# Kernel optimization log

Hardware: AMD Instinct MI355X
Metric: run time of the kernel (lower is better)

The kernel has to match this reference:

```python
import jax, jax.numpy as jnp
import numpy as np

GRID = 30
S = GRID * GRID            # 900 cells
D = 512                    # embed_dim
HQ = 8                     # query heads
HKV = 2                    # kv heads (GQA)
DH = D // HQ               # 64 head dim
T = 16                     # history length


def _rope_pairwise_1d(x, pos, inv_freq):
    """RoPE on adjacent pairs. x: (L,H,d), pos: (L,), inv_freq: (d//2,)."""
    theta = pos[:, None] * inv_freq[None, :]          # (L, d//2)
    cos = jnp.cos(theta)[:, None, :]                  # (L,1,d//2)
    sin = jnp.sin(theta)[:, None, :]
    xr, xi = x[..., 0::2], x[..., 1::2]               # even/odd pairs (= view(L,H,-1,2))
    out = jnp.stack((xr * cos - xi * sin, xr * sin + xi * cos), axis=-1)
    return out.reshape(x.shape)


def _rope_2d(x, coords_xy, inv_x, inv_y):
    """2D RoPE: first half rotated by x-coord, second half by y-coord."""
    d_axis = x.shape[-1] // 2
    x_part = _rope_pairwise_1d(x[..., :d_axis], coords_xy[:, 0], inv_x)
    y_part = _rope_pairwise_1d(x[..., d_axis:], coords_xy[:, 1], inv_y)
    return jnp.concatenate((x_part, y_part), axis=-1)


def setup_inputs() -> dict:
    key = jax.random.key(0)
    ks = jax.random.split(key, 7)
    sc = 1.0 / np.sqrt(D)
    return {
        "static_grid": jax.random.normal(ks[0], (GRID, GRID, D), jnp.float32),
        "history_seq": jax.random.normal(ks[1], (T, GRID, GRID, D), jnp.float32),
        "init_embed": jax.random.normal(ks[2], (D,), jnp.float32),
        "Wq": jax.random.normal(ks[3], (D, D), jnp.float32) * sc,
        "Wk": jax.random.normal(ks[4], (HKV * DH, D), jnp.float32) * sc,
        "Wv": jax.random.normal(ks[5], (HKV * DH, D), jnp.float32) * sc,
        "Wo": jax.random.normal(ks[6], (D, D), jnp.float32) * sc,
    }


def reference(static_grid, history_seq, init_embed, Wq, Wk, Wv, Wo):
    dtype = static_grid.dtype
    quarter, half = DH // 4, DH // 2
    inv_2d = 1.0 / (10000.0 ** (jnp.arange(quarter, dtype=dtype) / quarter))  # (dh//4,)
    inv_1d = 1.0 / (10000.0 ** (jnp.arange(half, dtype=dtype) / half))        # (dh//2,)

    gy, gx = jnp.meshgrid(jnp.arange(GRID), jnp.arange(GRID), indexing="ij")
    coords = jnp.stack((gy, gx), axis=-1).reshape(S, 2).astype(dtype)          # (S,2)

    cur = static_grid.reshape(S, D)                    # current frame tokens
    hist = history_seq.reshape(T * S, D)               # per-cell histories
    # token order: [learnable_init, cell_histories (t=0..T-1), current_grid]
    tokens = jnp.concatenate((init_embed[None, :], hist, cur), axis=0)  # (Lkv, D)

    tok_pos = jnp.concatenate((
        jnp.zeros((1,), dtype),
        jnp.repeat(jnp.arange(T, dtype=dtype), S),
        jnp.full((S,), T, dtype=dtype),
    ))                                                  # (Lkv,) temporal positions
    tok_coords = jnp.concatenate((
        jnp.zeros((1, 2), dtype),
        jnp.tile(coords, (T, 1)),
        coords,
    ), axis=0)                                          # (Lkv,2)

    # projections (queries only for the current frame; output is the updated frame)
    q = (cur @ Wq.T).reshape(S, HQ, DH)
    k = (tokens @ Wk.T).reshape(-1, HKV, DH)
    v = (tokens @ Wv.T).reshape(-1, HKV, DH)

    # fused temporal(1D) + spatial(2D) RoPE on q and k
    q = _rope_2d(_rope_pairwise_1d(q, jnp.full((S,), T, dtype=dtype), inv_1d), coords, inv_2d, inv_2d)
    k = _rope_2d(_rope_pairwise_1d(k, tok_pos, inv_1d), tok_coords, inv_2d, inv_2d)

    # grouped-query attention: expand kv heads
    g = HQ // HKV
    k = jnp.repeat(k, g, axis=1)                        # (Lkv, HQ, DH)
    v = jnp.repeat(v, g, axis=1)

    scores = jnp.einsum("qhd,khd->hqk", q, k) / jnp.sqrt(jnp.asarray(DH, dtype))

    # pedestal mask: attend to init + own temporal column + all current cells
    cell = jnp.arange(S)
    hist_cell = jnp.tile(cell, T)                       # (T*S,)
    mask = jnp.concatenate((
        jnp.ones((S, 1), bool),
        cell[:, None] == hist_cell[None, :],
        jnp.ones((S, S), bool),
    ), axis=1)                                          # (S, Lkv)
    scores = jnp.where(mask[None], scores, jnp.finfo(dtype).min)

    attn = jax.nn.softmax(scores, axis=-1)
    out = jnp.einsum("hqk,khd->qhd", attn, v).reshape(S, D)
    return (out @ Wo.T).reshape(GRID, GRID, D)
```

## Files before the change

### kernel.cpp

```cpp
#include <hip/hip_runtime.h>
#include <math.h>

static constexpr int GRIDN = 30;
static constexpr int S    = 900;
static constexpr int D    = 512;
static constexpr int HQ   = 8;
static constexpr int HKV  = 2;
static constexpr int T    = 16;
static constexpr int NTOK = 1 + T*S + S;
static constexpr int CUR0 = 1 + T*S;

static constexpr int THROWS = 15360;
static constexpr int VTC    = 960;
static constexpr int PBS    = 952;

typedef _Float16 half8  __attribute__((ext_vector_type(8)));
typedef _Float16 half4  __attribute__((ext_vector_type(4)));
typedef __fp16   fp16x2 __attribute__((ext_vector_type(2)));
typedef float    floatx4 __attribute__((ext_vector_type(4)));

#define MFMA16(a,b,c) __builtin_amdgcn_mfma_f32_16x16x32_f16((a),(b),(c),0,0,0)

#if defined(__has_builtin)
#if __has_builtin(__builtin_amdgcn_fdot2)
#define HAVE_FDOT2 1
#endif
#endif

__device__ __forceinline__ half8 to_half8(float4 a, float4 b) {
    half8 h;
    h[0]=(_Float16)a.x; h[1]=(_Float16)a.y; h[2]=(_Float16)a.z; h[3]=(_Float16)a.w;
    h[4]=(_Float16)b.x; h[5]=(_Float16)b.y; h[6]=(_Float16)b.z; h[7]=(_Float16)b.w;
    return h;
}

__device__ __forceinline__ half8 cvt8(float4 a, float4 b) {
    const fp16x2 p0 = __builtin_amdgcn_cvt_pkrtz(a.x, a.y);
    const fp16x2 p1 = __builtin_amdgcn_cvt_pkrtz(a.z, a.w);
    const fp16x2 p2 = __builtin_amdgcn_cvt_pkrtz(b.x, b.y);
    const fp16x2 p3 = __builtin_amdgcn_cvt_pkrtz(b.z, b.w);
    half8 h;
    h[0]=(_Float16)p0[0]; h[1]=(_Float16)p0[1];
    h[2]=(_Float16)p1[0]; h[3]=(_Float16)p1[1];
    h[4]=(_Float16)p2[0]; h[5]=(_Float16)p2[1];
    h[6]=(_Float16)p3[0]; h[7]=(_Float16)p3[1];
    return h;
}

__global__ __launch_bounds__(256) void prep_w(
    const float* __restrict__ Wq, const float* __restrict__ Wk,
    const float* __restrict__ Wv, const float* __restrict__ Wo,
    _Float16* __restrict__ Wqh, _Float16* __restrict__ Whkv,
    _Float16* __restrict__ Woh)
{
    const size_t i8 = ((size_t)blockIdx.x * 256 + threadIdx.x) * 8;
    const float* src; _Float16* dst; size_t off;
    if (i8 < 262144)      { src = Wq; dst = Wqh;          off = i8; }
    else if (i8 < 327680) { src = Wk; dst = Whkv;         off = i8 - 262144; }
    else if (i8 < 393216) { src = Wv; dst = Whkv + 65536; off = i8 - 327680; }
    else                  { src = Wo; dst = Woh;          off = i8 - 393216; }
    const float4 f0 = *(const float4*)(src + off);
    const float4 f1 = *(const float4*)(src + off + 4);
    *(half8*)(dst + off) = to_half8(f0, f1);
}

__global__ __launch_bounds__(256) void proj(
    const float* __restrict__ init_e, const float* __restrict__ hist,
    const float* __restrict__ cur,
    const _Float16* __restrict__ Whkv, const _Float16* __restrict__ Wqh,
    _Float16* __restrict__ Kh, _Float16* __restrict__ Vh,
    _Float16* __restrict__ Vt, _Float16* __restrict__ Qh)
{
    const int tid = threadIdx.x;
    const int w = tid >> 6, lane = tid & 63;
    const int r = lane & 15, kb = lane >> 4;
    const int bx = blockIdx.x;
    const bool isQ = (bx >= 479);

    int l0, n0;
    const _Float16* B;
    if (!isQ) { l0 = bx * 32; B = Whkv; n0 = 0; }
    else {
        const int qb = bx - 479;
        l0 = CUR0 + (qb >> 1) * 32;
        B = Wqh; n0 = (qb & 1) * 256;
    }

    const float* ap[2];
    #pragma unroll
    for (int mt = 0; mt < 2; ++mt) {
        int l = l0 + mt*16 + r;
        if (l >= NTOK) l = 0;
        const float* row = (l == 0) ? init_e
                         : (l <= T*S ? hist + (size_t)(l-1)*512
                                     : cur  + (size_t)(l-CUR0)*512);
        ap[mt] = row + kb*8;
    }
    const _Float16* bp[4];
    #pragma unroll
    for (int nt = 0; nt < 4; ++nt)
        bp[nt] = B + (size_t)(n0 + w*64 + nt*16 + r) * 512 + kb*8;

    floatx4 acc[2][4] = {};
    #pragma unroll 2
    for (int k0 = 0; k0 < 512; k0 += 32) {
        half8 a[2], b[4];
        #pragma unroll
        for (int mt = 0; mt < 2; ++mt) {
            const float4 f0 = *(const float4*)(ap[mt] + k0);
            const float4 f1 = *(const float4*)(ap[mt] + k0 + 4);
            a[mt] = cvt8(f0, f1);
        }
        #pragma unroll
        for (int nt = 0; nt < 4; ++nt) b[nt] = *(const half8*)(bp[nt] + k0);
        #pragma unroll
        for (int mt = 0; mt < 2; ++mt)
            #pragma unroll
            for (int nt = 0; nt < 4; ++nt)
                acc[mt][nt] = MFMA16(a[mt], b[nt], acc[mt][nt]);
    }

    const float LN1E4 = 9.210340371976184f;
    float inv1[4], inv2[4]; int jj[4];
    #pragma unroll
    for (int nt = 0; nt < 4; ++nt) {
        const int cl = nt*16 + r;
        jj[nt] = cl >> 1;
        inv1[nt] = __expf(-(float)jj[nt]        * (LN1E4 / 32.f));
        inv2[nt] = __expf(-(float)(jj[nt] & 15) * (LN1E4 / 16.f));
    }

    if (!isQ) {
        if (w < 2) {
            #pragma unroll
            for (int mt = 0; mt < 2; ++mt)
                #pragma unroll
                for (int i = 0; i < 4; ++i) {
                    const int l = l0 + mt*16 + kb*4 + i;
                    float pos, cy, cx;
                    if (l == 0) { pos = 0.f; cy = 0.f; cx = 0.f; }
                    else if (l <= T*S) {
                        const int j2 = l - 1;
                        const int t_ = j2 / S;
                        const int cell = j2 - t_ * S;
                        pos = (float)t_;
                        cy = (float)(cell / GRIDN); cx = (float)(cell % GRIDN);
                    } else {
                        const int cell = l - CUR0;
                        pos = (float)T;
                        cy = (float)(cell / GRIDN); cx = (float)(cell % GRIDN);
                    }
                    #pragma unroll
                    for (int nt = 0; nt < 4; ++nt) {
                        const float own = acc[mt][nt][i];
                        const float oth = __shfl_xor(own, 1);
                        const float c2 = (jj[nt] < 16) ? cy : cx;
                        const float theta = pos * inv1[nt] + c2 * inv2[nt];
                        float sn, cs; __sincosf(theta, &sn, &cs);
                        const int cl = nt*16 + r;
                        const float o = ((cl & 1) == 0) ? (own * cs - oth * sn)
                                                        : (oth * sn + own * cs);
                        if (l < NTOK) Kh[(size_t)l * 128 + w*64 + cl] = (_Float16)o;
                    }
                }
        } else {
            #pragma unroll
            for (int mt = 0; mt < 2; ++mt)
                #pragma unroll
                for (int nt = 0; nt < 4; ++nt) {
                    const int d = nt*16 + r;
                    #pragma unroll
                    for (int i = 0; i < 4; ++i) {
                        const int l = l0 + mt*16 + kb*4 + i;
                        if (l >= NTOK) continue;
                        const _Float16 hv = (_Float16)acc[mt][nt][i];
                        Vh[(size_t)l * 128 + (w-2)*64 + d] = hv;
                        const int cc = l - CUR0;
                        if (cc >= 0 && cc < S)
                            Vt[((size_t)(w-2)*64 + d) * VTC + cc] = hv;
                    }
                }
        }
    } else {
        #pragma unroll
        for (int mt = 0; mt < 2; ++mt)
            #pragma unroll
            for (int i = 0; i < 4; ++i) {
                const int l = l0 + mt*16 + kb*4 + i;
                const int s = l - CUR0;
                const float cy = (float)(s / GRIDN), cx = (float)(s % GRIDN);
                #pragma unroll
                for (int nt = 0; nt < 4; ++nt) {
                    const float own = acc[mt][nt][i];
                    const float oth = __shfl_xor(own, 1);
                    const float c2 = (jj[nt] < 16) ? cy : cx;
                    const float theta = 16.f * inv1[nt] + c2 * inv2[nt];
                    float sn, cs; __sincosf(theta, &sn, &cs);
                    const int cl = nt*16 + r;
                    const float o = ((cl & 1) == 0) ? (own * cs - oth * sn)
                                                    : (oth * sn + own * cs);
                    if (s < S)
                        Qh[(size_t)s * 512 + n0 + w*64 + cl] = (_Float16)(o * 0.125f);
                }
            }
    }
}

__global__ __launch_bounds__(256) void attn_f16(
    const _Float16* __restrict__ Qh, const _Float16* __restrict__ Kh,
    const _Float16* __restrict__ Vt, const _Float16* __restrict__ Vh,
    _Float16* __restrict__ Oh)
{
    __shared__ _Float16 pb[16][PBS];
    __shared__ float ex[16][20];
    __shared__ float wpm[4][16], wps[4][16];
    __shared__ float rowm[16], rowinv[16];
    __shared__ float Oe[16][68];

    const int q0  = blockIdx.x * 16;
    const int h   = blockIdx.y;
    const int kvh = h >> 2;
    const int tid = threadIdx.x;
    const int w = tid >> 6, lane = tid & 63;
    const int r = lane & 15, g = lane >> 4;

    {
        const int er = tid & 15;
        const int s  = q0 + er;
        const int ss = (s < S) ? s : 0;
        const _Float16* qp = Qh + (size_t)(q0 + er) * 512 + h * 64;
        for (int e = tid >> 4; e < 17; e += 16) {
            const int l = (e == 0) ? 0 : (1 + (e - 1) * S + ss);
            const _Float16* kp = Kh + (size_t)l * 128 + kvh * 64;
            float acc = 0.f;
            #pragma unroll
            for (int d8 = 0; d8 < 8; ++d8) {
                const half8 qv = *(const half8*)(qp + d8 * 8);
                const half8 kv = *(const half8*)(kp + d8 * 8);
#ifdef HAVE_FDOT2
                #pragma unroll
                for (int p_ = 0; p_ < 4; ++p_) {
                    fp16x2 qq; qq[0] = (__fp16)qv[2*p_]; qq[1] = (__fp16)qv[2*p_+1];
                    fp16x2 kk; kk[0] = (__fp16)kv[2*p_]; kk[1] = (__fp16)kv[2*p_+1];
                    acc = __builtin_amdgcn_fdot2(qq, kk, acc, false);
                }
#else
                #pragma unroll
                for (int q_ = 0; q_ < 8; ++q_)
                    acc += (float)qv[q_] * (float)kv[q_];
#endif
            }
            ex[er][e] = acc;
        }
    }

    half8 qa[2];
    #pragma unroll
    for (int ks = 0; ks < 2; ++ks)
        qa[ks] = *(const half8*)(Qh + (size_t)(q0 + r) * 512 + h * 64 + ks * 32 + g * 8);

    floatx4 qacc[15];
    #pragma unroll
    for (int t = 0; t < 15; ++t) {
        const int nt = w + 4 * t;
        floatx4 a = {0.f, 0.f, 0.f, 0.f};
        if (nt <= 56) {
            const _Float16* kp = Kh + (size_t)(CUR0 + nt * 16 + r) * 128 + kvh * 64 + g * 8;
            a = MFMA16(qa[0], *(const half8*)kp, a);
            a = MFMA16(qa[1], *(const half8*)(kp + 32), a);
        }
        qacc[t] = a;
    }

    float pm[4] = {-1e30f, -1e30f, -1e30f, -1e30f};
    #pragma unroll
    for (int t = 0; t < 15; ++t) {
        const int nt = w + 4 * t;
        const bool valid = (nt <= 56) && !((nt == 56) && (r >= 4));
        #pragma unroll
        for (int i = 0; i < 4; ++i)
            if (valid) pm[i] = fmaxf(pm[i], qacc[t][i]);
    }
    #pragma unroll
    for (int m = 1; m < 16; m <<= 1)
        #pragma unroll
        for (int i = 0; i < 4; ++i)
            pm[i] = fmaxf(pm[i], __shfl_xor(pm[i], m));
    if (r == 0)
        #pragma unroll
        for (int i = 0; i < 4; ++i) wpm[w][g * 4 + i] = pm[i];
    __syncthreads();

    if (tid < 16) {
        float m = fmaxf(fmaxf(wpm[0][tid], wpm[1][tid]), fmaxf(wpm[2][tid], wpm[3][tid]));
        #pragma unroll
        for (int e = 0; e < 17; ++e) m = fmaxf(m, ex[tid][e]);
        rowm[tid] = m;
    }
    __syncthreads();

    {
        const int er = tid & 15;
        for (int e = tid >> 4; e < 17; e += 16)
            ex[er][e] = __expf(ex[er][e] - rowm[er]);
    }
    pb[tid >> 4][912 + (tid & 15)] = (_Float16)0.f;

    float ps[4] = {0.f, 0.f, 0.f, 0.f};
    #pragma unroll
    for (int t = 0; t < 15; ++t) {
        const int nt = w + 4 * t;
        if (nt <= 56) {
            const int c = nt * 16 + r;
            const bool masked = (nt == 56) && (r >= 4);
            #pragma unroll
            for (int i = 0; i < 4; ++i) {
                const int row = g * 4 + i;
                const float e = masked ? 0.f : __expf(qacc[t][i] - rowm[row]);
                ps[i] += e;
                pb[row][c] = (_Float16)e;
            }
        }
    }
    #pragma unroll
    for (int m = 1; m < 16; m <<= 1)
        #pragma unroll
        for (int i = 0; i < 4; ++i) ps[i] += __shfl_xor(ps[i], m);
    if (r == 0)
        #pragma unroll
        for (int i = 0; i < 4; ++i) wps[w][g * 4 + i] = ps[i];
    __syncthreads();

    if (tid < 16) {
        float s_ = wps[0][tid] + wps[1][tid] + wps[2][tid] + wps[3][tid];
        #pragma unroll
        for (int e = 0; e < 17; ++e) s_ += ex[tid][e];
        rowinv[tid] = 1.f / s_;
    }
    __syncthreads();

    {
        const int er = tid & 15, gg = tid >> 4;
        const int s  = q0 + er;
        const int ss = (s < S) ? s : 0;
        float o0 = 0.f, o1 = 0.f, o2 = 0.f, o3 = 0.f;
        for (int e = 0; e < 17; ++e) {
            const int l = (e == 0) ? 0 : (1 + (e - 1) * S + ss);
            const float p = ex[er][e];
            const half4 v = *(const half4*)(Vh + (size_t)l * 128 + kvh * 64 + gg * 4);
            o0 = fmaf(p, (float)v[0], o0); o1 = fmaf(p, (float)v[1], o1);
            o2 = fmaf(p, (float)v[2], o2); o3 = fmaf(p, (float)v[3], o3);
        }
        *(float4*)&Oe[er][gg * 4] = make_float4(o0, o1, o2, o3);
    }

    const int d0 = w * 16;
    floatx4 oa = {0.f, 0.f, 0.f, 0.f};
    const _Float16* vrow = Vt + ((size_t)kvh * 64 + d0 + r) * VTC + g * 8;
    #pragma unroll
    for (int ks = 0; ks < 29; ++ks) {
        const half8 pf = *(const half8*)(&pb[r][ks * 32 + g * 8]);
        const half8 vf = *(const half8*)(vrow + ks * 32);
        oa = MFMA16(pf, vf, oa);
    }
    __syncthreads();

    #pragma unroll
    for (int i = 0; i < 4; ++i) {
        const int row = g * 4 + i;
        const int s = q0 + row;
        if (s < S) {
            const float o = (oa[i] + Oe[row][d0 + r]) * rowinv[row];
            Oh[(size_t)s * 512 + h * 64 + d0 + r] = (_Float16)o;
        }
    }
}

__global__ __launch_bounds__(256) void gemm_out(
    const _Float16* __restrict__ A, const _Float16* __restrict__ Wh,
    float* __restrict__ Out, int M)
{
    const int tid = threadIdx.x;
    const int w = tid >> 6, lane = tid & 63;
    const int r = lane & 15, kb = lane >> 4;
    const int l0 = blockIdx.x * 32;
    const int n0 = blockIdx.y * 256 + w*64;

    const _Float16* ap[2];
    #pragma unroll
    for (int mt = 0; mt < 2; ++mt)
        ap[mt] = A + (size_t)(l0 + mt*16 + r)*512 + kb*8;
    const _Float16* bp[4];
    #pragma unroll
    for (int nt = 0; nt < 4; ++nt)
        bp[nt] = Wh + (size_t)(n0 + nt*16 + r) * 512 + kb*8;

    floatx4 acc[2][4] = {};
    #pragma unroll 2
    for (int k0 = 0; k0 < 512; k0 += 32) {
        half8 a[2], b[4];
        #pragma unroll
        for (int mt = 0; mt < 2; ++mt) a[mt] = *(const half8*)(ap[mt] + k0);
        #pragma unroll
        for (int nt = 0; nt < 4; ++nt) b[nt] = *(const half8*)(bp[nt] + k0);
        #pragma unroll
        for (int mt = 0; mt < 2; ++mt)
            #pragma unroll
            for (int nt = 0; nt < 4; ++nt)
                acc[mt][nt] = MFMA16(a[mt], b[nt], acc[mt][nt]);
    }
    #pragma unroll
    for (int mt = 0; mt < 2; ++mt)
        #pragma unroll
        for (int nt = 0; nt < 4; ++nt)
            #pragma unroll
            for (int i = 0; i < 4; ++i) {
                const int l = l0 + mt*16 + kb*4 + i;
                if (l < M)
                    Out[(size_t)l*512 + n0 + nt*16 + r] = acc[mt][nt][i];
            }
}

extern "C" void kernel_launch(void* const* d_in, const int* in_sizes, int n_in,
                              void* d_out, int out_size, void* d_ws, size_t ws_size,
                              hipStream_t stream)
{
    (void)in_sizes; (void)n_in; (void)out_size; (void)ws_size;
    const float* static_grid = (const float*)d_in[0];
    const float* history     = (const float*)d_in[1];
    const float* init_embed  = (const float*)d_in[2];
    const float* Wq = (const float*)d_in[3];
    const float* Wk = (const float*)d_in[4];
    const float* Wv = (const float*)d_in[5];
    const float* Wo = (const float*)d_in[6];
    float* out = (float*)d_out;

    char* p = (char*)d_ws;
    _Float16* Wqh  = (_Float16*)p;  p += (size_t)262144 * 2;
    _Float16* Whkv = (_Float16*)p;  p += (size_t)131072 * 2;
    _Float16* Woh  = (_Float16*)p;  p += (size_t)262144 * 2;
    _Float16* Kh   = (_Float16*)p;  p += (size_t)THROWS * 128 * 2;
    _Float16* Vh   = (_Float16*)p;  p += (size_t)THROWS * 128 * 2;
    _Float16* Vt   = (_Float16*)p;  p += (size_t)2 * 64 * VTC * 2;
    _Float16* Qh   = (_Float16*)p;  p += (size_t)928 * 512 * 2;
    _Float16* Oh   = (_Float16*)p;  p += (size_t)928 * 512 * 2;

    prep_w<<<320, 256, 0, stream>>>(Wq, Wk, Wv, Wo, Wqh, Whkv, Woh);
    proj<<<537, 256, 0, stream>>>(init_embed, history, static_grid,
                                  Whkv, Wqh, Kh, Vh, Vt, Qh);
    attn_f16<<<dim3(57, 8), 256, 0, stream>>>(Qh, Kh, Vt, Vh, Oh);
    gemm_out<<<dim3(29, 2), 256, 0, stream>>>(Oh, Woh, out, S);
}
```

Measured before the change: 168.5 us.

## Stage projection GEMM tiles through double-buffered LDS with 64x128 block tiles

Rewrites the projection kernel so each block loads a 64-row by 128-column tile of activations and weights into double-buffered shared memory, converting fp32 activations to fp16 on the way, then feeds the MFMAs from LDS. Previously each wave read its A and B fragments straight from global memory, so activation rows were fetched redundantly by all four waves. The new tiling shares activation loads across waves and prefetches the next K-chunk while computing. The cost is extra LDS traffic, two barriers per chunk and a changed block-to-output mapping.

```diff
diff --git a/kernel.cpp b/kernel.cpp
--- a/kernel.cpp
+++ b/kernel.cpp
@@ -13,6 +13,7 @@
 static constexpr int THROWS = 15360;
 static constexpr int VTC    = 960;
 static constexpr int PBS    = 952;
+static constexpr int LSTR   = 72;
 
 typedef _Float16 half8  __attribute__((ext_vector_type(8)));
 typedef _Float16 half4  __attribute__((ext_vector_type(4)));
@@ -34,16 +35,12 @@
     return h;
 }
 
-__device__ __forceinline__ half8 cvt8(float4 a, float4 b) {
+__device__ __forceinline__ half4 cvt4(float4 a) {
     const fp16x2 p0 = __builtin_amdgcn_cvt_pkrtz(a.x, a.y);
     const fp16x2 p1 = __builtin_amdgcn_cvt_pkrtz(a.z, a.w);
-    const fp16x2 p2 = __builtin_amdgcn_cvt_pkrtz(b.x, b.y);
-    const fp16x2 p3 = __builtin_amdgcn_cvt_pkrtz(b.z, b.w);
-    half8 h;
+    half4 h;
     h[0]=(_Float16)p0[0]; h[1]=(_Float16)p0[1];
     h[2]=(_Float16)p1[0]; h[3]=(_Float16)p1[1];
-    h[4]=(_Float16)p2[0]; h[5]=(_Float16)p2[1];
-    h[6]=(_Float16)p3[0]; h[7]=(_Float16)p3[1];
     return h;
 }
 
@@ -71,72 +68,104 @@
     _Float16* __restrict__ Kh, _Float16* __restrict__ Vh,
     _Float16* __restrict__ Vt, _Float16* __restrict__ Qh)
 {
-    const int tid = threadIdx.x;
-    const int w = tid >> 6, lane = tid & 63;
-    const int r = lane & 15, kb = lane >> 4;
-    const int bx = blockIdx.x;
-    const bool isQ = (bx >= 479);
-
-    int l0, n0;
-    const _Float16* B;
-    if (!isQ) { l0 = bx * 32; B = Whkv; n0 = 0; }
-    else {
-        const int qb = bx - 479;
-        l0 = CUR0 + (qb >> 1) * 32;
-        B = Wqh; n0 = (qb & 1) * 256;
-    }
-
-    const float* ap[2];
-    #pragma unroll
-    for (int mt = 0; mt < 2; ++mt) {
-        int l = l0 + mt*16 + r;
+    __shared__ _Float16 Alds[2][64 * LSTR];
+    __shared__ _Float16 Blds[2][128 * LSTR];
+
+    const int tid  = threadIdx.x;
+    const int w    = tid >> 6, lane = tid & 63;
+    const int r    = lane & 15, kb = lane >> 4;
+    const int ww   = w >> 1, wc = w & 1;
+    const int bx   = blockIdx.x;
+    const bool isQ = (bx >= 480);
+
+    int l0, n0, bc;
+    const _Float16* Wb;
+    if (!isQ) { l0 = (bx >> 1) * 64;               bc = bx & 1;  n0 = bc * 128; Wb = Whkv; }
+    else      { const int qb = bx - 480;
+                l0 = CUR0 + (qb >> 2) * 64;        bc = qb & 3;  n0 = bc * 128; Wb = Wqh; }
+
+    const float* arow[4];
+    #pragma unroll
+    for (int j = 0; j < 4; ++j) {
+        int l = l0 + j * 16 + (tid >> 4);
         if (l >= NTOK) l = 0;
-        const float* row = (l == 0) ? init_e
-                         : (l <= T*S ? hist + (size_t)(l-1)*512
-                                     : cur  + (size_t)(l-CUR0)*512);
-        ap[mt] = row + kb*8;
-    }
-    const _Float16* bp[4];
-    #pragma unroll
-    for (int nt = 0; nt < 4; ++nt)
-        bp[nt] = B + (size_t)(n0 + w*64 + nt*16 + r) * 512 + kb*8;
+        const float* rp = (l == 0) ? init_e
+                        : (l <= T*S ? hist + (size_t)(l - 1) * 512
+                                    : cur  + (size_t)(l - CUR0) * 512);
+        arow[j] = rp + (tid & 15) * 4;
+    }
+    const _Float16* brow[4];
+    #pragma unroll
+    for (int j = 0; j < 4; ++j)
+        brow[j] = Wb + (size_t)(n0 + j * 32 + (tid >> 3)) * 512 + (tid & 7) * 8;
+
+    float4 areg[4];
+    half8  breg[4];
 
     floatx4 acc[2][4] = {};
-    #pragma unroll 2
-    for (int k0 = 0; k0 < 512; k0 += 32) {
-        half8 a[2], b[4];
-        #pragma unroll
-        for (int mt = 0; mt < 2; ++mt) {
-            const float4 f0 = *(const float4*)(ap[mt] + k0);
-            const float4 f1 = *(const float4*)(ap[mt] + k0 + 4);
-            a[mt] = cvt8(f0, f1);
-        }
-        #pragma unroll
-        for (int nt = 0; nt < 4; ++nt) b[nt] = *(const half8*)(bp[nt] + k0);
-        #pragma unroll
-        for (int mt = 0; mt < 2; ++mt)
+
+    #pragma unroll
+    for (int j = 0; j < 4; ++j) { areg[j] = *(const float4*)arow[j]; breg[j] = *(const half8*)brow[j]; }
+    #pragma unroll
+    for (int j = 0; j < 4; ++j) {
+        *(half4*)&Alds[0][(j*16 + (tid >> 4)) * LSTR + (tid & 15) * 4] = cvt4(areg[j]);
+        *(half8*)&Blds[0][(j*32 + (tid >> 3)) * LSTR + (tid & 7) * 8]  = breg[j];
+    }
+    __syncthreads();
+
+    for (int c = 0; c < 8; ++c) {
+        const int buf = c & 1;
+        if (c < 7) {
+            const int k0 = (c + 1) * 64;
+            #pragma unroll
+            for (int j = 0; j < 4; ++j) {
+                areg[j] = *(const float4*)(arow[j] + k0);
+                breg[j] = *(const half8*)(brow[j] + k0);
+            }
+        }
+        #pragma unroll
+        for (int s = 0; s < 2; ++s) {
+            half8 a[2], b[4];
+            #pragma unroll
+            for (int mt = 0; mt < 2; ++mt)
+                a[mt] = *(const half8*)&Alds[buf][(ww*32 + mt*16 + r) * LSTR + s*32 + kb*8];
             #pragma unroll
             for (int nt = 0; nt < 4; ++nt)
-                acc[mt][nt] = MFMA16(a[mt], b[nt], acc[mt][nt]);
+                b[nt] = *(const half8*)&Blds[buf][(wc*64 + nt*16 + r) * LSTR + s*32 + kb*8];
+            #pragma unroll
+            for (int mt = 0; mt < 2; ++mt)
+                #pragma unroll
+                for (int nt = 0; nt < 4; ++nt)
+                    acc[mt][nt] = MFMA16(a[mt], b[nt], acc[mt][nt]);
+        }
+        if (c < 7) {
+            __syncthreads();
+            #pragma unroll
+            for (int j = 0; j < 4; ++j) {
+                *(half4*)&Alds[buf ^ 1][(j*16 + (tid >> 4)) * LSTR + (tid & 15) * 4] = cvt4(areg[j]);
+                *(half8*)&Blds[buf ^ 1][(j*32 + (tid >> 3)) * LSTR + (tid & 7) * 8]  = breg[j];
+            }
+            __syncthreads();
+        }
     }
 
     const float LN1E4 = 9.210340371976184f;
     float inv1[4], inv2[4]; int jj[4];
     #pragma unroll
     for (int nt = 0; nt < 4; ++nt) {
-        const int cl = nt*16 + r;
+        const int cl = nt * 16 + r;
         jj[nt] = cl >> 1;
         inv1[nt] = __expf(-(float)jj[nt]        * (LN1E4 / 32.f));
         inv2[nt] = __expf(-(float)(jj[nt] & 15) * (LN1E4 / 16.f));
     }
 
     if (!isQ) {
-        if (w < 2) {
+        if (bc == 0) {
             #pragma unroll
             for (int mt = 0; mt < 2; ++mt)
                 #pragma unroll
                 for (int i = 0; i < 4; ++i) {
-                    const int l = l0 + mt*16 + kb*4 + i;
+                    const int l = l0 + ww*32 + mt*16 + kb*4 + i;
                     float pos, cy, cx;
                     if (l == 0) { pos = 0.f; cy = 0.f; cx = 0.f; }
                     else if (l <= T*S) {
@@ -157,10 +186,10 @@
                         const float c2 = (jj[nt] < 16) ? cy : cx;
                         const float theta = pos * inv1[nt] + c2 * inv2[nt];
                         float sn, cs; __sincosf(theta, &sn, &cs);
-                        const int cl = nt*16 + r;
-                        const float o = ((cl & 1) == 0) ? (own * cs - oth * sn)
+                        const int cc = wc*64 + nt*16 + r;
+                        const float o = ((cc & 1) == 0) ? (own * cs - oth * sn)
                                                         : (oth * sn + own * cs);
-                        if (l < NTOK) Kh[(size_t)l * 128 + w*64 + cl] = (_Float16)o;
+                        if (l < NTOK) Kh[(size_t)l * 128 + cc] = (_Float16)o;
                     }
                 }
         } else {
@@ -168,16 +197,16 @@
             for (int mt = 0; mt < 2; ++mt)
                 #pragma unroll
                 for (int nt = 0; nt < 4; ++nt) {
-                    const int d = nt*16 + r;
+                    const int vd = wc*64 + nt*16 + r;
                     #pragma unroll
                     for (int i = 0; i < 4; ++i) {
-                        const int l = l0 + mt*16 + kb*4 + i;
+                        const int l = l0 + ww*32 + mt*16 + kb*4 + i;
                         if (l >= NTOK) continue;
                         const _Float16 hv = (_Float16)acc[mt][nt][i];
-                        Vh[(size_t)l * 128 + (w-2)*64 + d] = hv;
+                        Vh[(size_t)l * 128 + vd] = hv;
                         const int cc = l - CUR0;
                         if (cc >= 0 && cc < S)
-                            Vt[((size_t)(w-2)*64 + d) * VTC + cc] = hv;
+                            Vt[(size_t)vd * VTC + cc] = hv;
                     }
                 }
         }
@@ -186,9 +215,10 @@
         for (int mt = 0; mt < 2; ++mt)
             #pragma unroll
             for (int i = 0; i < 4; ++i) {
-                const int l = l0 + mt*16 + kb*4 + i;
+                const int l = l0 + ww*32 + mt*16 + kb*4 + i;
                 const int s = l - CUR0;
-                const float cy = (float)(s / GRIDN), cx = (float)(s % GRIDN);
+                const int ssafe = (s < S) ? s : 0;
+                const float cy = (float)(ssafe / GRIDN), cx = (float)(ssafe % GRIDN);
                 #pragma unroll
                 for (int nt = 0; nt < 4; ++nt) {
                     const float own = acc[mt][nt][i];
@@ -196,11 +226,11 @@
                     const float c2 = (jj[nt] < 16) ? cy : cx;
                     const float theta = 16.f * inv1[nt] + c2 * inv2[nt];
                     float sn, cs; __sincosf(theta, &sn, &cs);
-                    const int cl = nt*16 + r;
-                    const float o = ((cl & 1) == 0) ? (own * cs - oth * sn)
-                                                    : (oth * sn + own * cs);
+                    const int C = bc*128 + wc*64 + nt*16 + r;
+                    const float o = ((C & 1) == 0) ? (own * cs - oth * sn)
+                                                   : (oth * sn + own * cs);
                     if (s < S)
-                        Qh[(size_t)s * 512 + n0 + w*64 + cl] = (_Float16)(o * 0.125f);
+                        Qh[(size_t)s * 512 + C] = (_Float16)(o * 0.125f);
                 }
             }
     }
@@ -446,7 +476,7 @@
     _Float16* Oh   = (_Float16*)p;  p += (size_t)928 * 512 * 2;
 
     prep_w<<<320, 256, 0, stream>>>(Wq, Wk, Wv, Wo, Wqh, Whkv, Woh);
-    proj<<<537, 256, 0, stream>>>(init_embed, history, static_grid,
+    proj<<<540, 256, 0, stream>>>(init_embed, history, static_grid,
                                   Whkv, Wqh, Kh, Vh, Vt, Qh);
     attn_f16<<<dim3(57, 8), 256, 0, stream>>>(Qh, Kh, Vt, Vh, Oh);
     gemm_out<<<dim3(29, 2), 256, 0, stream>>>(Oh, Woh, out, S);
```

New measurement: 144.9 us. 1.16x faster.
